# Performance work log

Hardware: AMD Instinct MI355X
Metric: run time of the kernel (lower is better)

The kernel has to match this reference:

```python
import jax, jax.numpy as jnp
import numpy as np
import math

NUM_HEADS = 8
DIM = 512
HEAD_DIM = DIM // NUM_HEADS
SCALE = HEAD_DIM ** -0.5
RP = 2            # remove_pad = kernel_size//2 * 2 for kernel_size=3
EPS_GN = 1e-5     # GroupNorm eps
EPS_L1 = 1e-12    # F.normalize eps


def _conv(x, w, b):
    # x: [B, Cin, H, W], w: [Cout, Cin, 3, 3] (OIHW), VALID padding, stride 1
    y = jax.lax.conv_general_dilated(x, w, (1, 1), 'VALID',
                                     dimension_numbers=('NCHW', 'OIHW', 'NCHW'))
    return y + b[None, :, None, None]


def _gn_per_channel(x, g, b):
    # GroupNorm with num_groups == num_channels: per-channel norm over (H, W)
    mu = x.mean(axis=(-2, -1), keepdims=True)
    var = x.var(axis=(-2, -1), keepdims=True)
    xn = (x - mu) * jax.lax.rsqrt(var + EPS_GN)
    return xn * g[None, :, None, None] + b[None, :, None, None]


def _ppe(rpe, c1w, c1b, g1w, g1b, c2w, c2b, g2w, g2b):
    # PeripheralPositionEncoding: rpe [side^2, side^2, 4*H] -> [1, H, N, N], N=(side-2*RP)^2
    nr, _, d = rpe.shape
    side = int(round(math.sqrt(nr)))
    s2 = side - 2 * RP
    x = rpe.reshape(side, side, side, side, d)          # i j k l d
    x = x[RP:side - RP, RP:side - RP]                   # trim i, j borders
    x = x.transpose(0, 1, 4, 2, 3).reshape(s2 * s2, d, side, side)  # (ij) d k l
    x = jax.nn.relu(_gn_per_channel(_conv(x, c1w, c1b), g1w, g1b))
    x = _gn_per_channel(_conv(x, c2w, c2b), g2w, g2b)   # [(ij), H, s2, s2]
    y = x.reshape(s2 * s2, NUM_HEADS, s2 * s2).transpose(1, 0, 2)[None]  # [1,H,N,N]
    return jax.nn.sigmoid(y)


def setup_inputs() -> dict:
    key = jax.random.key(0)
    ks = jax.random.split(key, 12)
    B, N = 8, 1024            # N = (36 - 4)^2
    side = 36
    cin = NUM_HEADS * 4       # 32
    inp = {
        'x': jax.random.normal(ks[0], (B, N, DIM), jnp.float32),
        'rpe_embed': jax.random.normal(ks[1], (side * side, side * side, cin), jnp.float32),
        'wqkv': jax.random.normal(ks[2], (3 * DIM, DIM), jnp.float32) * 0.02,
        'wproj': jax.random.normal(ks[3], (DIM, DIM), jnp.float32) * 0.02,
        'bproj': jnp.zeros((DIM,), jnp.float32),
        'c1w': jax.random.normal(ks[4], (cin, cin, 3, 3), jnp.float32) * 0.02,
        'c1b': jnp.zeros((cin,), jnp.float32),
        'g1w': jnp.ones((cin,), jnp.float32),
        'g1b': jnp.zeros((cin,), jnp.float32),
        'c2w': jax.random.normal(ks[5], (NUM_HEADS, cin, 3, 3), jnp.float32) * 0.02,
        'c2b': jnp.zeros((NUM_HEADS,), jnp.float32),
        'g2w': jnp.ones((NUM_HEADS,), jnp.float32),        # norm_init[1] = 1.0
        'g2b': jnp.zeros((NUM_HEADS,), jnp.float32),       # norm_init[0] = 0.0
    }
    return inp


def reference(x, rpe_embed, wqkv, wproj, bproj, c1w, c1b, g1w, g1b, c2w, c2b, g2w, g2b):
    B, N, D = x.shape
    H, HD = NUM_HEADS, HEAD_DIM
    qkv = x @ wqkv.T                                   # [B, N, 3D]
    q, k, v = jnp.split(qkv, 3, axis=-1)
    def heads(t):
        return t.reshape(B, N, H, HD).transpose(0, 2, 1, 3)  # [B, H, N, HD]
    q, k, v = heads(q), heads(k), heads(v)
    dots = jnp.einsum('bhnd,bhmd->bhnm', q, k) * SCALE
    dots = jnp.exp(dots - dots.max(axis=-1, keepdims=True))  # stable exp-score
    w = _ppe(rpe_embed, c1w, c1b, g1w, g1b, c2w, c2b, g2w, g2b)  # [1,H,N,N]
    attn = w * dots
    attn = attn / jnp.maximum(jnp.abs(attn).sum(axis=-1, keepdims=True), EPS_L1)  # L1 normalize
    out = jnp.einsum('bhnm,bhmd->bhnd', attn, v)
    out = out.transpose(0, 2, 1, 3).reshape(B, N, D)
    return out @ wproj.T + bproj
```

## Files before the change

### kernel.cpp

```cpp
#include <hip/hip_runtime.h>
#include <hip/hip_fp16.h>


typedef __attribute__((ext_vector_type(8))) short bf16x8;
typedef __attribute__((ext_vector_type(8))) _Float16 f16x8;
typedef __attribute__((ext_vector_type(4))) float f32x4;

__device__ __forceinline__ unsigned short f2bf(float f) {
  unsigned u = __builtin_bit_cast(unsigned, f);
  u += 0x7FFFu + ((u >> 16) & 1u);
  return (unsigned short)(u >> 16);
}

__global__ __launch_bounds__(256) void wprep(
    const float* __restrict__ c1w, const float* __restrict__ c2w,
    unsigned short* __restrict__ w1frag, unsigned short* __restrict__ w2frag)
{
  int t = blockIdx.x * 256 + threadIdx.x;
  if (t < 9216) {
    int j = t & 7, ln = (t >> 3) & 63, ctap = t >> 9;
    int tap = ctap >> 1, ct = ctap & 1;
    int oc = 2 * (ln & 15) + ct, ic = (ln >> 4) * 8 + j;
    w1frag[t] = __half_as_ushort(__float2half(c1w[(oc * 32 + ic) * 9 + tap]));
  }
  if (t < 4608) {
    int j = t & 7, ln = (t >> 3) & 63, tap = t >> 9;
    int oc = (ln & 15) & 7, ic = (ln >> 4) * 8 + j;
    w2frag[t] = __half_as_ushort(__float2half(c2w[(oc * 32 + ic) * 9 + tap]));
  }
}

__global__ __launch_bounds__(256) void cvt_all(
    const float* __restrict__ x, const float* __restrict__ wqkv,
    const float* __restrict__ wproj,
    __half* __restrict__ xh, __half* __restrict__ wqkvh, __half* __restrict__ wprojh)
{
  int t = blockIdx.x * 256 + threadIdx.x;
  const float4* srcp;
  __half* dstp;
  int idx;
  if (t < 1048576)      { srcp = (const float4*)x;     dstp = xh;     idx = t; }
  else if (t < 1245184) { srcp = (const float4*)wqkv;  dstp = wqkvh;  idx = t - 1048576; }
  else                  { srcp = (const float4*)wproj; dstp = wprojh; idx = t - 1245184; }
  float4 v = srcp[idx];
  __half2 h0 = __floats2half2_rn(v.x, v.y);
  __half2 h1 = __floats2half2_rn(v.z, v.w);
  uint2 u; u.x = __builtin_bit_cast(unsigned, h0); u.y = __builtin_bit_cast(unsigned, h1);
  *(uint2*)&dstp[idx * 4] = u;
}

template<bool OUT_BF16>
__global__ __launch_bounds__(256) void gemm_f16_bt(
    const __half* __restrict__ Ah, const __half* __restrict__ Bh,
    void* __restrict__ Cv, const float* __restrict__ bias,
    int M, int N, int K)
{
  __shared__ __align__(16) _Float16 As[128 * 40];
  __shared__ __align__(16) _Float16 Bs[128 * 40];
  const int tid = threadIdx.x;
  const int wv = tid >> 6, ln = tid & 63, lr = ln & 15, lq = ln >> 4;
  const int wm = wv >> 1, wn = wv & 1;
  const int m0 = blockIdx.y * 128, n0 = blockIdx.x * 128;

  f32x4 acc[4][4];
#pragma unroll
  for (int i = 0; i < 4; i++)
#pragma unroll
    for (int j = 0; j < 4; j++) acc[i][j] = (f32x4){0.f, 0.f, 0.f, 0.f};

  const int sr = tid >> 1, sk = (tid & 1) * 16;

  for (int k0 = 0; k0 < K; k0 += 32) {
    uint4 ha0 = *(const uint4*)(Ah + (size_t)(m0 + sr) * K + k0 + sk);
    uint4 ha1 = *(const uint4*)(Ah + (size_t)(m0 + sr) * K + k0 + sk + 8);
    uint4 hb0 = *(const uint4*)(Bh + (size_t)(n0 + sr) * K + k0 + sk);
    uint4 hb1 = *(const uint4*)(Bh + (size_t)(n0 + sr) * K + k0 + sk + 8);
    __syncthreads();
    *(uint4*)&As[sr * 40 + sk] = ha0;
    *(uint4*)&As[sr * 40 + sk + 8] = ha1;
    *(uint4*)&Bs[sr * 40 + sk] = hb0;
    *(uint4*)&Bs[sr * 40 + sk + 8] = hb1;
    __syncthreads();
    f16x8 af[4], bf[4];
#pragma unroll
    for (int mf = 0; mf < 4; mf++)
      af[mf] = *(const f16x8*)&As[(wm * 64 + mf * 16 + lr) * 40 + lq * 8];
#pragma unroll
    for (int nf = 0; nf < 4; nf++)
      bf[nf] = *(const f16x8*)&Bs[(wn * 64 + nf * 16 + lr) * 40 + lq * 8];
#pragma unroll
    for (int mf = 0; mf < 4; mf++)
#pragma unroll
      for (int nf = 0; nf < 4; nf++)
        acc[mf][nf] = __builtin_amdgcn_mfma_f32_16x16x32_f16(af[mf], bf[nf], acc[mf][nf], 0, 0, 0);
  }

#pragma unroll
  for (int mf = 0; mf < 4; mf++)
#pragma unroll
    for (int reg = 0; reg < 4; reg++) {
      const int row = m0 + wm * 64 + mf * 16 + lq * 4 + reg;
#pragma unroll
      for (int nf = 0; nf < 4; nf++) {
        const int col = n0 + wn * 64 + nf * 16 + lr;
        float v = acc[mf][nf][reg];
        if (bias) v += bias[col];
        if (OUT_BF16) ((unsigned short*)Cv)[(size_t)row * N + col] = f2bf(v);
        else          ((float*)Cv)[(size_t)row * N + col] = v;
      }
    }
}

__global__ __launch_bounds__(1024, 1) void conv_fused3(
    const float* __restrict__ rpe,
    const unsigned short* __restrict__ w1frag, const unsigned short* __restrict__ w2frag,
    const float* __restrict__ g1, const float* __restrict__ b1,
    const float* __restrict__ g2, const float* __restrict__ b2,
    __half* __restrict__ wout)
{
  extern __shared__ __align__(16) char smem[];
  unsigned short* inA = (unsigned short*)smem;
  unsigned short* yB  = (unsigned short*)(smem + 82944);
  float* statA = (float*)(smem + 156928);
  float* aL    = (float*)(smem + 157184);
  float* cL    = aL + 32;
  float* transF = (float*)smem;

  const int tid = threadIdx.x;
  const int wv = tid >> 6, ln = tid & 63;
  const int lr = ln & 15, lq = ln >> 4;
  const int p = blockIdx.x;

  if (tid < 64) statA[tid] = 0.f;

  const float* src = rpe + (size_t)(((p >> 5) + 2) * 36 + (p & 31) + 2) * 41472;
  for (int t = tid; t < 10368; t += 1024) {
    int pix = t >> 3, dq = (t & 7) << 2;
    float4 v = *(const float4*)(src + pix * 32 + dq);
    __half2 h0 = __floats2half2_rn(v.x, v.y);
    __half2 h1 = __floats2half2_rn(v.z, v.w);
    uint2 u; u.x = __builtin_bit_cast(unsigned, h0); u.y = __builtin_bit_cast(unsigned, h1);
    *(uint2*)&inA[(dq >> 3) * 10368 + pix * 8 + (dq & 7)] = u;
  }

  f16x8 w1f[2][9];
#pragma unroll
  for (int ct = 0; ct < 2; ct++)
#pragma unroll
    for (int tap = 0; tap < 9; tap++)
      w1f[ct][tap] = *(const f16x8*)&w1frag[((tap * 2 + ct) * 64 + ln) * 8];
  __syncthreads();

  constexpr int OFF1[9] = {0, 8, 16, 288, 296, 304, 576, 584, 592};
  const unsigned short* inAg = inA + lq * 10368;
  float s0 = 0.f, q0 = 0.f, s1 = 0.f, q1 = 0.f;
  for (int t0 = wv; t0 < 64; t0 += 32) {
    const int tA = t0, tB = t0 + 16;
    const int mA = tA * 16 + lr, mB = tB * 16 + lr;
    const unsigned short* abA = inAg + ((mA / 34) * 36 + (mA % 34)) * 8;
    const unsigned short* abB = inAg + ((mB / 34) * 36 + (mB % 34)) * 8;
    f32x4 cA0 = {0.f,0.f,0.f,0.f}, cA1 = {0.f,0.f,0.f,0.f};
    f32x4 cB0 = {0.f,0.f,0.f,0.f}, cB1 = {0.f,0.f,0.f,0.f};
#pragma unroll
    for (int tap = 0; tap < 9; tap++) {
      f16x8 avA = *(const f16x8*)(abA + OFF1[tap]);
      f16x8 avB = *(const f16x8*)(abB + OFF1[tap]);
      cA0 = __builtin_amdgcn_mfma_f32_16x16x32_f16(avA, w1f[0][tap], cA0, 0, 0, 0);
      cA1 = __builtin_amdgcn_mfma_f32_16x16x32_f16(avA, w1f[1][tap], cA1, 0, 0, 0);
      cB0 = __builtin_amdgcn_mfma_f32_16x16x32_f16(avB, w1f[0][tap], cB0, 0, 0, 0);
      cB1 = __builtin_amdgcn_mfma_f32_16x16x32_f16(avB, w1f[1][tap], cB1, 0, 0, 0);
    }
#pragma unroll
    for (int r = 0; r < 4; r++) {
      int moA = tA * 16 + lq * 4 + r;
      float v0 = cA0[r], v1 = cA1[r];
      unsigned u = (unsigned)__half_as_ushort(__float2half(v0))
                 | ((unsigned)__half_as_ushort(__float2half(v1)) << 16);
      *(unsigned*)&yB[(lr >> 2) * 9248 + moA * 8 + ((lr * 2) & 7)] = u;
      s0 += v0; q0 += v0 * v0; s1 += v1; q1 += v1 * v1;
      int moB = tB * 16 + lq * 4 + r;
      float w0 = cB0[r], w1 = cB1[r];
      unsigned u2 = (unsigned)__half_as_ushort(__float2half(w0))
                  | ((unsigned)__half_as_ushort(__float2half(w1)) << 16);
      *(unsigned*)&yB[(lr >> 2) * 9248 + moB * 8 + ((lr * 2) & 7)] = u2;
      s0 += w0; q0 += w0 * w0; s1 += w1; q1 += w1 * w1;
    }
  }
  if (wv < 9) {
    int t = wv + 64;
    int m = t * 16 + lr;
    int ms = m < 1155 ? m : 1155;
    const unsigned short* ab = inAg + ((ms / 34) * 36 + (ms % 34)) * 8;
    f32x4 c0 = {0.f,0.f,0.f,0.f}, c1v = {0.f,0.f,0.f,0.f};
#pragma unroll
    for (int tap = 0; tap < 9; tap++) {
      f16x8 av = *(const f16x8*)(ab + OFF1[tap]);
      c0  = __builtin_amdgcn_mfma_f32_16x16x32_f16(av, w1f[0][tap], c0, 0, 0, 0);
      c1v = __builtin_amdgcn_mfma_f32_16x16x32_f16(av, w1f[1][tap], c1v, 0, 0, 0);
    }
#pragma unroll
    for (int r = 0; r < 4; r++) {
      int mo = t * 16 + lq * 4 + r;
      if (mo < 1156) {
        float v0 = c0[r], v1 = c1v[r];
        unsigned u = (unsigned)__half_as_ushort(__float2half(v0))
                   | ((unsigned)__half_as_ushort(__float2half(v1)) << 16);
        *(unsigned*)&yB[(lr >> 2) * 9248 + mo * 8 + ((lr * 2) & 7)] = u;
        s0 += v0; q0 += v0 * v0; s1 += v1; q1 += v1 * v1;
      }
    }
  }
#pragma unroll
  for (int off = 16; off < 64; off <<= 1) {
    s0 += __shfl_xor(s0, off); q0 += __shfl_xor(q0, off);
    s1 += __shfl_xor(s1, off); q1 += __shfl_xor(q1, off);
  }
  if (ln < 16) {
    atomicAdd(&statA[ln], s0);      atomicAdd(&statA[16 + ln], q0);
    atomicAdd(&statA[32 + ln], s1); atomicAdd(&statA[48 + ln], q1);
  }
  __syncthreads();
  if (tid < 32) {
    int cti = tid >> 4, lri = tid & 15;
    float s = statA[cti * 32 + lri];
    float q = statA[cti * 32 + 16 + lri];
    int ch = 2 * lri + cti;
    float mu = s * (1.f / 1156.f);
    float var = q * (1.f / 1156.f) - mu * mu;
    float a_ = rsqrtf(var + 1e-5f) * g1[ch];
    aL[ch] = a_; cL[ch] = b1[ch] - mu * a_;
  }
  if (tid < 16) statA[tid] = 0.f;
  __syncthreads();

  {
    int g = tid >> 8, ocb = g * 8;
    unsigned short* yg = yB + g * 9248;
    for (int pix = (tid & 255); pix < 1156; pix += 256) {
      f16x8 raw = *(const f16x8*)&yg[pix * 8];
      f16x8 outv;
#pragma unroll
      for (int e = 0; e < 8; e++) {
        float v = (float)raw[e];
        outv[e] = (_Float16)fmaxf(v * aL[ocb + e] + cL[ocb + e], 0.f);
      }
      *(f16x8*)&yg[pix * 8] = outv;
    }
  }
  __syncthreads();

  f16x8 w2f[9];
#pragma unroll
  for (int tap = 0; tap < 9; tap++)
    w2f[tap] = *(const f16x8*)&w2frag[(tap * 64 + ln) * 8];

  constexpr int OFF2[9] = {0, 8, 16, 272, 280, 288, 544, 552, 560};
  const unsigned short* yBg = yB + lq * 9248;
  float s2 = 0.f, q2 = 0.f;
#pragma unroll
  for (int t0 = 0; t0 < 2; t0++) {
    const int tA = wv + t0 * 32, tB = tA + 16;
    const int mA = tA * 16 + lr, mB = tB * 16 + lr;
    const unsigned short* abA = yBg + ((mA >> 5) * 34 + (mA & 31)) * 8;
    const unsigned short* abB = yBg + ((mB >> 5) * 34 + (mB & 31)) * 8;
    f32x4 ccA = {0.f,0.f,0.f,0.f}, ccB = {0.f,0.f,0.f,0.f};
#pragma unroll
    for (int tap = 0; tap < 9; tap++) {
      f16x8 avA = *(const f16x8*)(abA + OFF2[tap]);
      f16x8 avB = *(const f16x8*)(abB + OFF2[tap]);
      ccA = __builtin_amdgcn_mfma_f32_16x16x32_f16(avA, w2f[tap], ccA, 0, 0, 0);
      ccB = __builtin_amdgcn_mfma_f32_16x16x32_f16(avB, w2f[tap], ccB, 0, 0, 0);
    }
#pragma unroll
    for (int r = 0; r < 4; r++) {
      float vA = ccA[r], vB = ccB[r];
      s2 += vA + vB; q2 += vA * vA + vB * vB;
      if (lr < 8) {
        transF[lr * 1032 + tA * 16 + lq * 4 + r] = vA;
        transF[lr * 1032 + tB * 16 + lq * 4 + r] = vB;
      }
    }
  }
#pragma unroll
  for (int off = 16; off < 64; off <<= 1) {
    s2 += __shfl_xor(s2, off); q2 += __shfl_xor(q2, off);
  }
  if (ln < 8) { atomicAdd(&statA[ln], s2); atomicAdd(&statA[8 + ln], q2); }
  __syncthreads();
  if (tid < 8) {
    float s = statA[tid], q = statA[8 + tid];
    float mu = s * (1.f / 1024.f);
    float var = q * (1.f / 1024.f) - mu * mu;
    float a_ = rsqrtf(var + 1e-5f) * g2[tid];
    aL[tid] = a_; cL[tid] = b2[tid] - mu * a_;
  }
  __syncthreads();

  {
    int oc = tid >> 7, p8 = (tid & 127) << 3;
    float a_ = aL[oc], c_ = cL[oc];
    f16x8 o;
#pragma unroll
    for (int e = 0; e < 8; e++) {
      float v = transF[oc * 1032 + p8 + e];
      o[e] = (_Float16)(1.f / (1.f + __expf(-(v * a_ + c_))));
    }
    *(f16x8*)&wout[((size_t)oc << 20) + ((size_t)p << 10) + p8] = o;
  }
}

__global__ __launch_bounds__(256) void attn_kernel(
    const unsigned short* __restrict__ qkv,
    const __half* __restrict__ wppe,
    __half* __restrict__ oh)
{
  __shared__ __align__(16) unsigned short k_lds[64 * 72];
  __shared__ __align__(16) unsigned short v_lds[64 * 72];
  __shared__ __align__(16) unsigned short p_lds[4 * 16 * 72];
  const int tid = threadIdx.x;
  const int wv = tid >> 6, ln = tid & 63;
  const int lr = ln & 15, lq = ln >> 4;
  const int b = blockIdx.y >> 3, h = blockIdx.y & 7;
  const int n0 = blockIdx.x << 6;

  const size_t qoff = (size_t)((b << 10) + n0 + (wv << 4) + lr) * 1536 + (h << 6);
  bf16x8 qf0 = *(const bf16x8*)(qkv + qoff + lq * 8);
  bf16x8 qf1 = *(const bf16x8*)(qkv + qoff + 32 + lq * 8);

  f32x4 acc[4];
#pragma unroll
  for (int dt = 0; dt < 4; dt++) acc[dt] = (f32x4){0.f, 0.f, 0.f, 0.f};
  float den[4] = {0.f, 0.f, 0.f, 0.f};
  const __half* wp = wppe + ((size_t)h << 20);

  for (int m0 = 0; m0 < 1024; m0 += 64) {
    __syncthreads();
    float wpre[4][4];
#pragma unroll
    for (int mt = 0; mt < 4; mt++)
#pragma unroll
      for (int reg = 0; reg < 4; reg++)
        wpre[mt][reg] = __half2float(
            wp[(size_t)(n0 + (wv << 4) + lq * 4 + reg) * 1024 + (m0 + mt * 16 + lr)]);
    for (int t = tid; t < 512; t += 256) {
      int m = t >> 3, dq = t & 7;
      const unsigned short* kr = qkv + (size_t)((b << 10) + m0 + m) * 1536 + 512 + (h << 6) + dq * 8;
      *(uint4*)&k_lds[m * 72 + dq * 8] = *(const uint4*)kr;
      uint4 vvv = *(const uint4*)(kr + 512);
      unsigned short tmp[8];
      *(uint4*)tmp = vvv;
#pragma unroll
      for (int i = 0; i < 8; i++) {
        int d = dq * 8 + i;
        v_lds[d * 72 + (m ^ (((d >> 3) & 7) << 3))] = tmp[i];
      }
    }
    __syncthreads();

    f32x4 s[4];
#pragma unroll
    for (int mt = 0; mt < 4; mt++) {
      const unsigned short* kb = &k_lds[(mt * 16 + lr) * 72 + lq * 8];
      f32x4 cz = (f32x4){0.f, 0.f, 0.f, 0.f};
      cz = __builtin_amdgcn_mfma_f32_16x16x32_bf16(qf0, *(const bf16x8*)kb, cz, 0, 0, 0);
      cz = __builtin_amdgcn_mfma_f32_16x16x32_bf16(qf1, *(const bf16x8*)(kb + 32), cz, 0, 0, 0);
      s[mt] = cz;
    }
#pragma unroll
    for (int mt = 0; mt < 4; mt++)
#pragma unroll
      for (int reg = 0; reg < 4; reg++) {
        int rrow = lq * 4 + reg;
        float pv = wpre[mt][reg] * __expf(s[mt][reg] * 0.125f);
        den[reg] += pv;
        p_lds[((wv << 4) + rrow) * 72 + mt * 16 + lr] = f2bf(pv);
      }
    const unsigned short* pb = &p_lds[((wv << 4) + lr) * 72];
    bf16x8 pa0 = *(const bf16x8*)(pb + lq * 8);
    bf16x8 pa1 = *(const bf16x8*)(pb + 32 + lq * 8);
#pragma unroll
    for (int dt = 0; dt < 4; dt++) {
      int d = dt * 16 + lr;
      int sw = ((d >> 3) & 7) << 3;
      const unsigned short* vb = &v_lds[d * 72];
      acc[dt] = __builtin_amdgcn_mfma_f32_16x16x32_bf16(pa0, *(const bf16x8*)(vb + ((lq * 8) ^ sw)), acc[dt], 0, 0, 0);
      acc[dt] = __builtin_amdgcn_mfma_f32_16x16x32_bf16(pa1, *(const bf16x8*)(vb + ((32 + lq * 8) ^ sw)), acc[dt], 0, 0, 0);
    }
  }
#pragma unroll
  for (int off = 1; off < 16; off <<= 1)
#pragma unroll
    for (int reg = 0; reg < 4; reg++) den[reg] += __shfl_xor(den[reg], off);
#pragma unroll
  for (int dt = 0; dt < 4; dt++)
#pragma unroll
    for (int reg = 0; reg < 4; reg++) {
      size_t row = (size_t)((b << 10) + n0 + (wv << 4) + lq * 4 + reg);
      oh[row * 512 + (h << 6) + dt * 16 + lr] = __float2half(acc[dt][reg] / den[reg]);
    }
}

extern "C" void kernel_launch(void* const* d_in, const int* in_sizes, int n_in,
                              void* d_out, int out_size, void* d_ws, size_t ws_size,
                              hipStream_t stream) {
  (void)in_sizes; (void)n_in; (void)out_size; (void)ws_size;
  const float* x     = (const float*)d_in[0];
  const float* rpe   = (const float*)d_in[1];
  const float* wqkv  = (const float*)d_in[2];
  const float* wproj = (const float*)d_in[3];
  const float* bproj = (const float*)d_in[4];
  const float* c1w   = (const float*)d_in[5];
  const float* g1w   = (const float*)d_in[7];
  const float* g1b   = (const float*)d_in[8];
  const float* c2w   = (const float*)d_in[9];
  const float* g2w   = (const float*)d_in[11];
  const float* g2b   = (const float*)d_in[12];
  float* out = (float*)d_out;

  char* ws = (char*)d_ws;
  unsigned short* qkv_bf = (unsigned short*)ws;
  __half* wppe_h = (__half*)(ws + 25165824);
  __half* oh_h   = (__half*)(ws + 41943040);
  unsigned short* w1frag = (unsigned short*)(ws + 50331648);
  unsigned short* w2frag = (unsigned short*)(ws + 50350080);
  __half* wqkvh  = (__half*)(ws + 50359296);
  __half* wprojh = (__half*)(ws + 51932160);
  __half* xh     = (__half*)(ws + 52456448);

  wprep<<<36, 256, 0, stream>>>(c1w, c2w, w1frag, w2frag);
  cvt_all<<<5120, 256, 0, stream>>>(x, wqkv, wproj, xh, wqkvh, wprojh);

  gemm_f16_bt<true><<<dim3(12, 64), 256, 0, stream>>>(
      xh, wqkvh, qkv_bf, nullptr, 8192, 1536, 512);

  const int ldsC = 157440;
  hipFuncSetAttribute(reinterpret_cast<const void*>(&conv_fused3),
                      hipFuncAttributeMaxDynamicSharedMemorySize, ldsC);
  conv_fused3<<<1024, 1024, ldsC, stream>>>(rpe, w1frag, w2frag, g1w, g1b, g2w, g2b, wppe_h);

  attn_kernel<<<dim3(16, 64), 256, 0, stream>>>(qkv_bf, wppe_h, oh_h);

  gemm_f16_bt<false><<<dim3(4, 64), 256, 0, stream>>>(
      oh_h, wprojh, out, bproj, 8192, 512, 512);
}
```

Measured before the change: 193.2 us.

## Make conv kernel persistent with register-staged prefetch of next RPE slice

The fused PPE conv kernel now launches 256 persistent blocks, each handling 4 positions in a loop. While conv1 runs on the current slice, the next position's fp32 RPE slice is loaded into registers and written to LDS as fp16 after conv1 finishes, overlapping global loads with MFMA work. To make room, the conv2 transpose buffer moves to the yB region and results are held in registers until the stats barrier. The cost is higher register pressure (44 extra VGPRs for staging) and fewer blocks than CUs, which may leave some CUs idle.

```diff
diff --git a/kernel.cpp b/kernel.cpp
--- a/kernel.cpp
+++ b/kernel.cpp
@@ -111,7 +111,7 @@
     }
 }
 
-__global__ __launch_bounds__(1024, 1) void conv_fused3(
+__global__ __launch_bounds__(1024, 1) void conv_fused5(
     const float* __restrict__ rpe,
     const unsigned short* __restrict__ w1frag, const unsigned short* __restrict__ w2frag,
     const float* __restrict__ g1, const float* __restrict__ b1,
@@ -124,188 +124,232 @@
   float* statA = (float*)(smem + 156928);
   float* aL    = (float*)(smem + 157184);
   float* cL    = aL + 32;
-  float* transF = (float*)smem;
+  float* transF = (float*)(smem + 82944);
 
   const int tid = threadIdx.x;
   const int wv = tid >> 6, ln = tid & 63;
   const int lr = ln & 15, lq = ln >> 4;
-  const int p = blockIdx.x;
 
   if (tid < 64) statA[tid] = 0.f;
 
-  const float* src = rpe + (size_t)(((p >> 5) + 2) * 36 + (p & 31) + 2) * 41472;
-  for (int t = tid; t < 10368; t += 1024) {
-    int pix = t >> 3, dq = (t & 7) << 2;
-    float4 v = *(const float4*)(src + pix * 32 + dq);
-    __half2 h0 = __floats2half2_rn(v.x, v.y);
-    __half2 h1 = __floats2half2_rn(v.z, v.w);
-    uint2 u; u.x = __builtin_bit_cast(unsigned, h0); u.y = __builtin_bit_cast(unsigned, h1);
-    *(uint2*)&inA[(dq >> 3) * 10368 + pix * 8 + (dq & 7)] = u;
-  }
-
-  f16x8 w1f[2][9];
-#pragma unroll
-  for (int ct = 0; ct < 2; ct++)
-#pragma unroll
-    for (int tap = 0; tap < 9; tap++)
-      w1f[ct][tap] = *(const f16x8*)&w1frag[((tap * 2 + ct) * 64 + ln) * 8];
+  {
+    const int p = blockIdx.x;
+    const float* src = rpe + (size_t)(((p >> 5) + 2) * 36 + (p & 31) + 2) * 41472;
+    for (int e = tid; e < 10368; e += 1024) {
+      float4 v = *(const float4*)(src + e * 4);
+      __half2 h0 = __floats2half2_rn(v.x, v.y);
+      __half2 h1 = __floats2half2_rn(v.z, v.w);
+      uint2 u; u.x = __builtin_bit_cast(unsigned, h0); u.y = __builtin_bit_cast(unsigned, h1);
+      *(uint2*)&inA[((e & 7) >> 1) * 10368 + (e >> 3) * 8 + (e & 1) * 4] = u;
+    }
+  }
   __syncthreads();
 
   constexpr int OFF1[9] = {0, 8, 16, 288, 296, 304, 576, 584, 592};
+  constexpr int OFF2[9] = {0, 8, 16, 272, 280, 288, 544, 552, 560};
   const unsigned short* inAg = inA + lq * 10368;
-  float s0 = 0.f, q0 = 0.f, s1 = 0.f, q1 = 0.f;
-  for (int t0 = wv; t0 < 64; t0 += 32) {
-    const int tA = t0, tB = t0 + 16;
-    const int mA = tA * 16 + lr, mB = tB * 16 + lr;
-    const unsigned short* abA = inAg + ((mA / 34) * 36 + (mA % 34)) * 8;
-    const unsigned short* abB = inAg + ((mB / 34) * 36 + (mB % 34)) * 8;
-    f32x4 cA0 = {0.f,0.f,0.f,0.f}, cA1 = {0.f,0.f,0.f,0.f};
-    f32x4 cB0 = {0.f,0.f,0.f,0.f}, cB1 = {0.f,0.f,0.f,0.f};
-#pragma unroll
-    for (int tap = 0; tap < 9; tap++) {
-      f16x8 avA = *(const f16x8*)(abA + OFF1[tap]);
-      f16x8 avB = *(const f16x8*)(abB + OFF1[tap]);
-      cA0 = __builtin_amdgcn_mfma_f32_16x16x32_f16(avA, w1f[0][tap], cA0, 0, 0, 0);
-      cA1 = __builtin_amdgcn_mfma_f32_16x16x32_f16(avA, w1f[1][tap], cA1, 0, 0, 0);
-      cB0 = __builtin_amdgcn_mfma_f32_16x16x32_f16(avB, w1f[0][tap], cB0, 0, 0, 0);
-      cB1 = __builtin_amdgcn_mfma_f32_16x16x32_f16(avB, w1f[1][tap], cB1, 0, 0, 0);
-    }
-#pragma unroll
-    for (int r = 0; r < 4; r++) {
-      int moA = tA * 16 + lq * 4 + r;
-      float v0 = cA0[r], v1 = cA1[r];
-      unsigned u = (unsigned)__half_as_ushort(__float2half(v0))
-                 | ((unsigned)__half_as_ushort(__float2half(v1)) << 16);
-      *(unsigned*)&yB[(lr >> 2) * 9248 + moA * 8 + ((lr * 2) & 7)] = u;
-      s0 += v0; q0 += v0 * v0; s1 += v1; q1 += v1 * v1;
-      int moB = tB * 16 + lq * 4 + r;
-      float w0 = cB0[r], w1 = cB1[r];
-      unsigned u2 = (unsigned)__half_as_ushort(__float2half(w0))
-                  | ((unsigned)__half_as_ushort(__float2half(w1)) << 16);
-      *(unsigned*)&yB[(lr >> 2) * 9248 + moB * 8 + ((lr * 2) & 7)] = u2;
-      s0 += w0; q0 += w0 * w0; s1 += w1; q1 += w1 * w1;
-    }
-  }
-  if (wv < 9) {
-    int t = wv + 64;
-    int m = t * 16 + lr;
-    int ms = m < 1155 ? m : 1155;
-    const unsigned short* ab = inAg + ((ms / 34) * 36 + (ms % 34)) * 8;
-    f32x4 c0 = {0.f,0.f,0.f,0.f}, c1v = {0.f,0.f,0.f,0.f};
-#pragma unroll
-    for (int tap = 0; tap < 9; tap++) {
-      f16x8 av = *(const f16x8*)(ab + OFF1[tap]);
-      c0  = __builtin_amdgcn_mfma_f32_16x16x32_f16(av, w1f[0][tap], c0, 0, 0, 0);
-      c1v = __builtin_amdgcn_mfma_f32_16x16x32_f16(av, w1f[1][tap], c1v, 0, 0, 0);
-    }
-#pragma unroll
-    for (int r = 0; r < 4; r++) {
-      int mo = t * 16 + lq * 4 + r;
-      if (mo < 1156) {
-        float v0 = c0[r], v1 = c1v[r];
+  const unsigned short* yBg  = yB + lq * 9248;
+
+  for (int it = 0; it < 4; ++it) {
+    const int p = blockIdx.x + (it << 8);
+
+    float4 stg[11];
+    if (it < 3) {
+      const int pn = p + 256;
+      const float* srcn = rpe + (size_t)(((pn >> 5) + 2) * 36 + (pn & 31) + 2) * 41472;
+#pragma unroll
+      for (int k = 0; k < 10; k++) stg[k] = *(const float4*)(srcn + (tid + k * 1024) * 4);
+      if (tid < 128) stg[10] = *(const float4*)(srcn + (tid + 10240) * 4);
+    }
+
+    f16x8 w1f[2][9];
+#pragma unroll
+    for (int ct = 0; ct < 2; ct++)
+#pragma unroll
+      for (int tap = 0; tap < 9; tap++)
+        w1f[ct][tap] = *(const f16x8*)&w1frag[((tap * 2 + ct) * 64 + ln) * 8];
+
+    float s0 = 0.f, q0 = 0.f, s1 = 0.f, q1 = 0.f;
+    for (int t0 = wv; t0 < 64; t0 += 32) {
+      const int tA = t0, tB = t0 + 16;
+      const int mA = tA * 16 + lr, mB = tB * 16 + lr;
+      const unsigned short* abA = inAg + ((mA / 34) * 36 + (mA % 34)) * 8;
+      const unsigned short* abB = inAg + ((mB / 34) * 36 + (mB % 34)) * 8;
+      f32x4 cA0 = {0.f,0.f,0.f,0.f}, cA1 = {0.f,0.f,0.f,0.f};
+      f32x4 cB0 = {0.f,0.f,0.f,0.f}, cB1 = {0.f,0.f,0.f,0.f};
+#pragma unroll
+      for (int tap = 0; tap < 9; tap++) {
+        f16x8 avA = *(const f16x8*)(abA + OFF1[tap]);
+        f16x8 avB = *(const f16x8*)(abB + OFF1[tap]);
+        cA0 = __builtin_amdgcn_mfma_f32_16x16x32_f16(avA, w1f[0][tap], cA0, 0, 0, 0);
+        cA1 = __builtin_amdgcn_mfma_f32_16x16x32_f16(avA, w1f[1][tap], cA1, 0, 0, 0);
+        cB0 = __builtin_amdgcn_mfma_f32_16x16x32_f16(avB, w1f[0][tap], cB0, 0, 0, 0);
+        cB1 = __builtin_amdgcn_mfma_f32_16x16x32_f16(avB, w1f[1][tap], cB1, 0, 0, 0);
+      }
+#pragma unroll
+      for (int r = 0; r < 4; r++) {
+        int moA = tA * 16 + lq * 4 + r;
+        float v0 = cA0[r], v1 = cA1[r];
         unsigned u = (unsigned)__half_as_ushort(__float2half(v0))
                    | ((unsigned)__half_as_ushort(__float2half(v1)) << 16);
-        *(unsigned*)&yB[(lr >> 2) * 9248 + mo * 8 + ((lr * 2) & 7)] = u;
+        *(unsigned*)&yB[(lr >> 2) * 9248 + moA * 8 + ((lr * 2) & 7)] = u;
         s0 += v0; q0 += v0 * v0; s1 += v1; q1 += v1 * v1;
-      }
-    }
-  }
-#pragma unroll
-  for (int off = 16; off < 64; off <<= 1) {
-    s0 += __shfl_xor(s0, off); q0 += __shfl_xor(q0, off);
-    s1 += __shfl_xor(s1, off); q1 += __shfl_xor(q1, off);
-  }
-  if (ln < 16) {
-    atomicAdd(&statA[ln], s0);      atomicAdd(&statA[16 + ln], q0);
-    atomicAdd(&statA[32 + ln], s1); atomicAdd(&statA[48 + ln], q1);
-  }
-  __syncthreads();
-  if (tid < 32) {
-    int cti = tid >> 4, lri = tid & 15;
-    float s = statA[cti * 32 + lri];
-    float q = statA[cti * 32 + 16 + lri];
-    int ch = 2 * lri + cti;
-    float mu = s * (1.f / 1156.f);
-    float var = q * (1.f / 1156.f) - mu * mu;
-    float a_ = rsqrtf(var + 1e-5f) * g1[ch];
-    aL[ch] = a_; cL[ch] = b1[ch] - mu * a_;
-  }
-  if (tid < 16) statA[tid] = 0.f;
-  __syncthreads();
-
-  {
-    int g = tid >> 8, ocb = g * 8;
-    unsigned short* yg = yB + g * 9248;
-    for (int pix = (tid & 255); pix < 1156; pix += 256) {
-      f16x8 raw = *(const f16x8*)&yg[pix * 8];
-      f16x8 outv;
+        int moB = tB * 16 + lq * 4 + r;
+        float w0 = cB0[r], w1 = cB1[r];
+        unsigned u2 = (unsigned)__half_as_ushort(__float2half(w0))
+                    | ((unsigned)__half_as_ushort(__float2half(w1)) << 16);
+        *(unsigned*)&yB[(lr >> 2) * 9248 + moB * 8 + ((lr * 2) & 7)] = u2;
+        s0 += w0; q0 += w0 * w0; s1 += w1; q1 += w1 * w1;
+      }
+    }
+    if (wv < 9) {
+      int t = wv + 64;
+      int m = t * 16 + lr;
+      int ms = m < 1155 ? m : 1155;
+      const unsigned short* ab = inAg + ((ms / 34) * 36 + (ms % 34)) * 8;
+      f32x4 c0 = {0.f,0.f,0.f,0.f}, c1v = {0.f,0.f,0.f,0.f};
+#pragma unroll
+      for (int tap = 0; tap < 9; tap++) {
+        f16x8 av = *(const f16x8*)(ab + OFF1[tap]);
+        c0  = __builtin_amdgcn_mfma_f32_16x16x32_f16(av, w1f[0][tap], c0, 0, 0, 0);
+        c1v = __builtin_amdgcn_mfma_f32_16x16x32_f16(av, w1f[1][tap], c1v, 0, 0, 0);
+      }
+#pragma unroll
+      for (int r = 0; r < 4; r++) {
+        int mo = t * 16 + lq * 4 + r;
+        if (mo < 1156) {
+          float v0 = c0[r], v1 = c1v[r];
+          unsigned u = (unsigned)__half_as_ushort(__float2half(v0))
+                     | ((unsigned)__half_as_ushort(__float2half(v1)) << 16);
+          *(unsigned*)&yB[(lr >> 2) * 9248 + mo * 8 + ((lr * 2) & 7)] = u;
+          s0 += v0; q0 += v0 * v0; s1 += v1; q1 += v1 * v1;
+        }
+      }
+    }
+#pragma unroll
+    for (int off = 16; off < 64; off <<= 1) {
+      s0 += __shfl_xor(s0, off); q0 += __shfl_xor(q0, off);
+      s1 += __shfl_xor(s1, off); q1 += __shfl_xor(q1, off);
+    }
+    if (ln < 16) {
+      atomicAdd(&statA[ln], s0);      atomicAdd(&statA[16 + ln], q0);
+      atomicAdd(&statA[32 + ln], s1); atomicAdd(&statA[48 + ln], q1);
+    }
+    __syncthreads();
+
+    if (it < 3) {
+#pragma unroll
+      for (int k = 0; k < 10; k++) {
+        int e = tid + k * 1024;
+        __half2 h0 = __floats2half2_rn(stg[k].x, stg[k].y);
+        __half2 h1 = __floats2half2_rn(stg[k].z, stg[k].w);
+        uint2 u; u.x = __builtin_bit_cast(unsigned, h0); u.y = __builtin_bit_cast(unsigned, h1);
+        *(uint2*)&inA[((e & 7) >> 1) * 10368 + (e >> 3) * 8 + (e & 1) * 4] = u;
+      }
+      if (tid < 128) {
+        int e = tid + 10240;
+        __half2 h0 = __floats2half2_rn(stg[10].x, stg[10].y);
+        __half2 h1 = __floats2half2_rn(stg[10].z, stg[10].w);
+        uint2 u; u.x = __builtin_bit_cast(unsigned, h0); u.y = __builtin_bit_cast(unsigned, h1);
+        *(uint2*)&inA[((e & 7) >> 1) * 10368 + (e >> 3) * 8 + (e & 1) * 4] = u;
+      }
+    }
+    if (tid < 32) {
+      int cti = tid >> 4, lri = tid & 15;
+      float s = statA[cti * 32 + lri];
+      float q = statA[cti * 32 + 16 + lri];
+      int ch = 2 * lri + cti;
+      float mu = s * (1.f / 1156.f);
+      float var = q * (1.f / 1156.f) - mu * mu;
+      float a_ = rsqrtf(var + 1e-5f) * g1[ch];
+      aL[ch] = a_; cL[ch] = b1[ch] - mu * a_;
+    }
+    if (tid < 16) statA[tid] = 0.f;
+    __syncthreads();
+
+    {
+      int g = tid >> 8, ocb = g * 8;
+      unsigned short* yg = yB + g * 9248;
+      for (int pix = (tid & 255); pix < 1156; pix += 256) {
+        f16x8 raw = *(const f16x8*)&yg[pix * 8];
+        f16x8 outv;
+#pragma unroll
+        for (int e = 0; e < 8; e++) {
+          float v = (float)raw[e];
+          outv[e] = (_Float16)fmaxf(v * aL[ocb + e] + cL[ocb + e], 0.f);
+        }
+        *(f16x8*)&yg[pix * 8] = outv;
+      }
+    }
+    __syncthreads();
+
+    f16x8 w2f[9];
+#pragma unroll
+    for (int tap = 0; tap < 9; tap++)
+      w2f[tap] = *(const f16x8*)&w2frag[(tap * 64 + ln) * 8];
+
+    f32x4 zsave[4];
+    float s2 = 0.f, q2 = 0.f;
+#pragma unroll
+    for (int t0 = 0; t0 < 2; t0++) {
+      const int tA = wv + t0 * 32, tB = tA + 16;
+      const int mA = tA * 16 + lr, mB = tB * 16 + lr;
+      const unsigned short* abA = yBg + ((mA >> 5) * 34 + (mA & 31)) * 8;
+      const unsigned short* abB = yBg + ((mB >> 5) * 34 + (mB & 31)) * 8;
+      f32x4 ccA = {0.f,0.f,0.f,0.f}, ccB = {0.f,0.f,0.f,0.f};
+#pragma unroll
+      for (int tap = 0; tap < 9; tap++) {
+        f16x8 avA = *(const f16x8*)(abA + OFF2[tap]);
+        f16x8 avB = *(const f16x8*)(abB + OFF2[tap]);
+        ccA = __builtin_amdgcn_mfma_f32_16x16x32_f16(avA, w2f[tap], ccA, 0, 0, 0);
+        ccB = __builtin_amdgcn_mfma_f32_16x16x32_f16(avB, w2f[tap], ccB, 0, 0, 0);
+      }
+      zsave[t0 * 2] = ccA; zsave[t0 * 2 + 1] = ccB;
+#pragma unroll
+      for (int r = 0; r < 4; r++) {
+        s2 += ccA[r] + ccB[r]; q2 += ccA[r] * ccA[r] + ccB[r] * ccB[r];
+      }
+    }
+#pragma unroll
+    for (int off = 16; off < 64; off <<= 1) {
+      s2 += __shfl_xor(s2, off); q2 += __shfl_xor(q2, off);
+    }
+    if (ln < 8) { atomicAdd(&statA[ln], s2); atomicAdd(&statA[8 + ln], q2); }
+    __syncthreads();
+
+    if (lr < 8) {
+#pragma unroll
+      for (int t0 = 0; t0 < 2; t0++) {
+        const int tA = wv + t0 * 32, tB = tA + 16;
+#pragma unroll
+        for (int r = 0; r < 4; r++) {
+          transF[lr * 1032 + tA * 16 + lq * 4 + r] = zsave[t0 * 2][r];
+          transF[lr * 1032 + tB * 16 + lq * 4 + r] = zsave[t0 * 2 + 1][r];
+        }
+      }
+    }
+    if (tid < 8) {
+      float s = statA[tid], q = statA[8 + tid];
+      float mu = s * (1.f / 1024.f);
+      float var = q * (1.f / 1024.f) - mu * mu;
+      float a_ = rsqrtf(var + 1e-5f) * g2[tid];
+      aL[tid] = a_; cL[tid] = b2[tid] - mu * a_;
+    }
+    __syncthreads();
+
+    {
+      int oc = tid >> 7, p8 = (tid & 127) << 3;
+      float a_ = aL[oc], c_ = cL[oc];
+      f16x8 o;
 #pragma unroll
       for (int e = 0; e < 8; e++) {
-        float v = (float)raw[e];
-        outv[e] = (_Float16)fmaxf(v * aL[ocb + e] + cL[ocb + e], 0.f);
-      }
-      *(f16x8*)&yg[pix * 8] = outv;
-    }
-  }
-  __syncthreads();
-
-  f16x8 w2f[9];
-#pragma unroll
-  for (int tap = 0; tap < 9; tap++)
-    w2f[tap] = *(const f16x8*)&w2frag[(tap * 64 + ln) * 8];
-
-  constexpr int OFF2[9] = {0, 8, 16, 272, 280, 288, 544, 552, 560};
-  const unsigned short* yBg = yB + lq * 9248;
-  float s2 = 0.f, q2 = 0.f;
-#pragma unroll
-  for (int t0 = 0; t0 < 2; t0++) {
-    const int tA = wv + t0 * 32, tB = tA + 16;
-    const int mA = tA * 16 + lr, mB = tB * 16 + lr;
-    const unsigned short* abA = yBg + ((mA >> 5) * 34 + (mA & 31)) * 8;
-    const unsigned short* abB = yBg + ((mB >> 5) * 34 + (mB & 31)) * 8;
-    f32x4 ccA = {0.f,0.f,0.f,0.f}, ccB = {0.f,0.f,0.f,0.f};
-#pragma unroll
-    for (int tap = 0; tap < 9; tap++) {
-      f16x8 avA = *(const f16x8*)(abA + OFF2[tap]);
-      f16x8 avB = *(const f16x8*)(abB + OFF2[tap]);
-      ccA = __builtin_amdgcn_mfma_f32_16x16x32_f16(avA, w2f[tap], ccA, 0, 0, 0);
-      ccB = __builtin_amdgcn_mfma_f32_16x16x32_f16(avB, w2f[tap], ccB, 0, 0, 0);
-    }
-#pragma unroll
-    for (int r = 0; r < 4; r++) {
-      float vA = ccA[r], vB = ccB[r];
-      s2 += vA + vB; q2 += vA * vA + vB * vB;
-      if (lr < 8) {
-        transF[lr * 1032 + tA * 16 + lq * 4 + r] = vA;
-        transF[lr * 1032 + tB * 16 + lq * 4 + r] = vB;
-      }
-    }
-  }
-#pragma unroll
-  for (int off = 16; off < 64; off <<= 1) {
-    s2 += __shfl_xor(s2, off); q2 += __shfl_xor(q2, off);
-  }
-  if (ln < 8) { atomicAdd(&statA[ln], s2); atomicAdd(&statA[8 + ln], q2); }
-  __syncthreads();
-  if (tid < 8) {
-    float s = statA[tid], q = statA[8 + tid];
-    float mu = s * (1.f / 1024.f);
-    float var = q * (1.f / 1024.f) - mu * mu;
-    float a_ = rsqrtf(var + 1e-5f) * g2[tid];
-    aL[tid] = a_; cL[tid] = b2[tid] - mu * a_;
-  }
-  __syncthreads();
-
-  {
-    int oc = tid >> 7, p8 = (tid & 127) << 3;
-    float a_ = aL[oc], c_ = cL[oc];
-    f16x8 o;
-#pragma unroll
-    for (int e = 0; e < 8; e++) {
-      float v = transF[oc * 1032 + p8 + e];
-      o[e] = (_Float16)(1.f / (1.f + __expf(-(v * a_ + c_))));
-    }
-    *(f16x8*)&wout[((size_t)oc << 20) + ((size_t)p << 10) + p8] = o;
+        float v = transF[oc * 1032 + p8 + e];
+        o[e] = (_Float16)(1.f / (1.f + __expf(-(v * a_ + c_))));
+      }
+      *(f16x8*)&wout[((size_t)oc << 20) + ((size_t)p << 10) + p8] = o;
+    }
+    if (tid < 64) statA[tid] = 0.f;
+    __syncthreads();
   }
 }
 
@@ -434,9 +478,9 @@
       xh, wqkvh, qkv_bf, nullptr, 8192, 1536, 512);
 
   const int ldsC = 157440;
-  hipFuncSetAttribute(reinterpret_cast<const void*>(&conv_fused3),
+  hipFuncSetAttribute(reinterpret_cast<const void*>(&conv_fused5),
                       hipFuncAttributeMaxDynamicSharedMemorySize, ldsC);
-  conv_fused3<<<1024, 1024, ldsC, stream>>>(rpe, w1frag, w2frag, g1w, g1b, g2w, g2b, wppe_h);
+  conv_fused5<<<256, 1024, ldsC, stream>>>(rpe, w1frag, w2frag, g1w, g1b, g2w, g2b, wppe_h);
 
   attn_kernel<<<dim3(16, 64), 256, 0, stream>>>(qkv_bf, wppe_h, oh_h);
 
```

Measured after the change: 290.8 us. 50.5% more time.
